# Performance work log

Hardware: AMD Instinct MI355X
Metric: run time of the kernel (lower is better)

## Reference

```python
import jax, jax.numpy as jnp
import numpy as np

B, S, E = 4, 2048, 1024
H = 16
HD = E // H  # head_dim = 64


def setup_inputs() -> dict:
    key = jax.random.key(0)
    ks = jax.random.split(key, 12)
    sc = 0.02
    return {
        "q_encodings": jax.random.normal(ks[0], (B, S, E), jnp.float32),
        "k_encodings": jax.random.normal(ks[1], (B, S, E), jnp.float32),
        "v_encodings": jax.random.normal(ks[2], (B, S, E), jnp.float32),
        # per-head q/k/v linear weights [H, HD, HD] and biases [H, HD]
        "Wq": jax.random.normal(ks[3], (H, HD, HD), jnp.float32) * sc,
        "bq": jax.random.normal(ks[4], (H, HD), jnp.float32) * sc,
        "Wk": jax.random.normal(ks[5], (H, HD, HD), jnp.float32) * sc,
        "bk": jax.random.normal(ks[6], (H, HD), jnp.float32) * sc,
        "Wv": jax.random.normal(ks[7], (H, HD, HD), jnp.float32) * sc,
        "bv": jax.random.normal(ks[8], (H, HD), jnp.float32) * sc,
        # output projection [E, E] + bias [E]
        "Wp": jax.random.normal(ks[9], (E, E), jnp.float32) * sc,
        "bp": jax.random.normal(ks[10], (E,), jnp.float32) * sc,
        "mask": 1,
    }


def reference(q_encodings, k_encodings, v_encodings, Wq, bq, Wk, bk, Wv, bv, Wp, bp, mask):
    b, s, e = q_encodings.shape
    h, hd, _ = Wq.shape
    split = lambda x: x.reshape(b, s, h, hd)  # per-head slices of n_embd
    # batched per-head linear projections (original loops over heads)
    Q = jnp.einsum('bshd,hde->bshe', split(q_encodings), Wq) + bq
    K = jnp.einsum('bshd,hde->bshe', split(k_encodings), Wk) + bk
    V = jnp.einsum('bshd,hde->bshe', split(v_encodings), Wv) + bv
    # scaled dot-product scores [B,H,S,S]; scale uses head_dim (Attention.n_embd)
    scores = jnp.einsum('bqhd,bkhd->bhqk', Q, K) / jnp.sqrt(jnp.float32(hd))
    if mask:  # static Python flag, matches torch `if mask:`
        causal = jnp.tril(jnp.ones((s, s), jnp.float32))
        scores = scores + jnp.where(causal == 0, jnp.float32(-jnp.inf), jnp.float32(0.0))
    attn = jax.nn.softmax(scores, axis=-1)
    ctx = jnp.einsum('bhqk,bkhd->bqhd', attn, V).reshape(b, s, e)
    return ctx @ Wp + bp
```

## Files before the change

### kernel.cpp

```cpp
#include <hip/hip_runtime.h>
#include <hip/hip_bf16.h>
#include <math.h>

typedef __bf16 bf16;
typedef __bf16 bf16x8 __attribute__((ext_vector_type(8)));
typedef float f32x4 __attribute__((ext_vector_type(4)));
typedef unsigned int u32x2 __attribute__((ext_vector_type(2)));

constexpr int B = 4, S = 2048, E = 1024, H = 16, HD = 64;

constexpr float QSCALE = 0.125f * 1.44269504088896340736f;
constexpr float DTHR = 11.5f;

static __device__ __forceinline__ float exp2_fast(float x) {
#if __has_builtin(__builtin_amdgcn_exp2f)
    return __builtin_amdgcn_exp2f(x);
#else
    float r; asm("v_exp_f32 %0, %1" : "=v"(r) : "v"(x)); return r;
#endif
}

static __device__ __forceinline__ unsigned pk_bf16(float a, float b) {
    union { bf16 h[2]; unsigned u; } r;
    r.h[0] = (bf16)a; r.h[1] = (bf16)b;
    return r.u;
}

static __device__ __forceinline__ float max3(float a, float b, float c) {
    return fmaxf(fmaxf(a, b), c);
}

static __device__ __forceinline__ void gl16(const void* g, void* l) {
    __builtin_amdgcn_global_load_lds(
        (__attribute__((address_space(1))) void*)g,
        (__attribute__((address_space(3))) void*)l,
        16, 0, 0);
}

__global__ __launch_bounds__(256) void prep_weights(
    const float* __restrict__ Wq, const float* __restrict__ Wk,
    const float* __restrict__ Wv, const float* __restrict__ Wp,
    bf16* __restrict__ Wt, bf16* __restrict__ Wpt)
{
    __shared__ float t[64][65];
    const int tid = threadIdx.x;
    const int x = blockIdx.x, y = blockIdx.y;
    if (y < 3) {
        const int h = x, p = y;
        const float* W = (p == 0) ? Wq : (p == 1) ? Wk : Wv;
        const float scale = (p == 0) ? QSCALE : 1.0f;
        #pragma unroll
        for (int i = 0; i < 16; ++i) {
            int idx = tid + i * 256;
            int d = idx >> 6, e = idx & 63;
            t[d][e] = W[(size_t)h * 4096 + d * 64 + e];
        }
        __syncthreads();
        bf16* dst = Wt + ((size_t)p * H + h) * 4096;
        #pragma unroll
        for (int i = 0; i < 16; ++i) {
            int idx = tid + i * 256;
            int e = idx >> 6, d = idx & 63;
            dst[e * 64 + d] = (bf16)(t[d][e] * scale);
        }
    } else {
        const int k0 = (y - 3) * 64, n0 = x * 64;
        #pragma unroll
        for (int i = 0; i < 16; ++i) {
            int idx = tid + i * 256;
            int r = idx >> 6, c = idx & 63;
            t[r][c] = Wp[(size_t)(k0 + r) * E + n0 + c];
        }
        __syncthreads();
        #pragma unroll
        for (int i = 0; i < 16; ++i) {
            int idx = tid + i * 256;
            int r = idx >> 6, c = idx & 63;
            Wpt[(size_t)(n0 + r) * E + k0 + c] = (bf16)t[c][r];
        }
    }
}

__global__ __launch_bounds__(256) void qkv_proj(
    const float* __restrict__ xq, const float* __restrict__ xk, const float* __restrict__ xv,
    const bf16* __restrict__ Wt,
    const float* __restrict__ bq, const float* __restrict__ bk, const float* __restrict__ bv,
    bf16* __restrict__ Qb, bf16* __restrict__ Kb, bf16* __restrict__ Vt)
{
    const int b = blockIdx.z, h = blockIdx.y, s0 = blockIdx.x * 128;
    const int tid = threadIdx.x;
    const int w = tid >> 6, l = tid & 63;
    const int l16 = l & 15, lg = l >> 4;
    const size_t bh = (size_t)b * H + h;

    __shared__ __align__(16) bf16 xs[128][64];
    __shared__ __align__(16) bf16 Wl[64][64];
    __shared__ __align__(16) bf16 ts[10240];

    const int r8 = l >> 3;
    const int wchunk = ((l & 7) ^ r8) * 8;

    for (int p = 0; p < 3; ++p) {
        const float* x    = (p == 0) ? xq : (p == 1) ? xk : xv;
        const float* bias = (p == 0) ? bq : (p == 1) ? bk : bv;
        const float  bsc  = (p == 0) ? QSCALE : 1.0f;

        __syncthreads();
        const bf16* wsrc = Wt + ((size_t)p * H + h) * 4096;
        #pragma unroll
        for (int i = 0; i < 2; ++i) {
            const int rb = 8 * (w + 4 * i);
            gl16(wsrc + (size_t)(rb + r8) * 64 + wchunk, &Wl[rb][0]);
        }
        #pragma unroll
        for (int i = 0; i < 4; ++i) {
            int idx = tid + i * 256;
            int r = idx >> 3, g = idx & 7;
            const float* src = &x[((size_t)b * S + s0 + r) * E + h * 64 + g * 8];
            float4 f0 = *(const float4*)src;
            float4 f1 = *(const float4*)(src + 4);
            union { bf16 h8[8]; uint4 u; } pk;
            pk.h8[0] = (bf16)f0.x; pk.h8[1] = (bf16)f0.y;
            pk.h8[2] = (bf16)f0.z; pk.h8[3] = (bf16)f0.w;
            pk.h8[4] = (bf16)f1.x; pk.h8[5] = (bf16)f1.y;
            pk.h8[6] = (bf16)f1.z; pk.h8[7] = (bf16)f1.w;
            *(uint4*)&xs[r][(g ^ (r & 7)) * 8] = pk.u;
        }
        __syncthreads();

        if (p < 2) {
            float bcol[4];
            #pragma unroll
            for (int ei = 0; ei < 4; ++ei)
                bcol[ei] = bias[h * 64 + ei * 16 + l16] * bsc;
            #pragma unroll
            for (int st = 0; st < 2; ++st) {
                const int srow = w * 32 + st * 16 + l16;
                bf16x8 a0 = *(const bf16x8*)&xs[srow][((lg    ) ^ (srow & 7)) * 8];
                bf16x8 a1 = *(const bf16x8*)&xs[srow][((4 + lg) ^ (srow & 7)) * 8];
                #pragma unroll
                for (int ei = 0; ei < 4; ++ei) {
                    const int erow = ei * 16 + l16;
                    bf16x8 b0 = *(const bf16x8*)&Wl[erow][((lg    ) ^ (erow & 7)) * 8];
                    bf16x8 b1 = *(const bf16x8*)&Wl[erow][((4 + lg) ^ (erow & 7)) * 8];
                    f32x4 acc = {0.f, 0.f, 0.f, 0.f};
                    acc = __builtin_amdgcn_mfma_f32_16x16x32_bf16(a0, b0, acc, 0, 0, 0);
                    acc = __builtin_amdgcn_mfma_f32_16x16x32_bf16(a1, b1, acc, 0, 0, 0);
                    #pragma unroll
                    for (int r = 0; r < 4; ++r)
                        ts[(w * 32 + st * 16 + 4 * lg + r) * 80 + ei * 16 + l16] =
                            (bf16)(acc[r] + bcol[ei]);
                }
            }
            __syncthreads();
            bf16* out = (p == 0) ? Qb : Kb;
            #pragma unroll
            for (int i = 0; i < 4; ++i) {
                int idx = tid + i * 256;
                int r = idx >> 3, g = idx & 7;
                uint4 v = *(const uint4*)&ts[r * 80 + g * 8];
                *(uint4*)(out + (bh * S + s0 + r) * 64 + g * 8) = v;
            }
        } else {
            float brow[4];
            #pragma unroll
            for (int r = 0; r < 4; ++r)
                brow[r] = bias[h * 64 + w * 16 + 4 * lg + r];
            const int erow = w * 16 + l16;
            bf16x8 a0 = *(const bf16x8*)&Wl[erow][((lg    ) ^ (erow & 7)) * 8];
            bf16x8 a1 = *(const bf16x8*)&Wl[erow][((4 + lg) ^ (erow & 7)) * 8];
            #pragma unroll
            for (int st = 0; st < 8; ++st) {
                const int srow = st * 16 + l16;
                bf16x8 b0 = *(const bf16x8*)&xs[srow][((lg    ) ^ (srow & 7)) * 8];
                bf16x8 b1 = *(const bf16x8*)&xs[srow][((4 + lg) ^ (srow & 7)) * 8];
                f32x4 acc = {0.f, 0.f, 0.f, 0.f};
                acc = __builtin_amdgcn_mfma_f32_16x16x32_bf16(a0, b0, acc, 0, 0, 0);
                acc = __builtin_amdgcn_mfma_f32_16x16x32_bf16(a1, b1, acc, 0, 0, 0);
                #pragma unroll
                for (int r = 0; r < 4; ++r)
                    ts[(w * 16 + 4 * lg + r) * 136 + st * 16 + l16] =
                        (bf16)(acc[r] + brow[r]);
            }
            __syncthreads();
            #pragma unroll
            for (int i = 0; i < 4; ++i) {
                int idx = tid + i * 256;
                int r = idx >> 4, g = idx & 15;
                uint4 v = *(const uint4*)&ts[r * 136 + g * 8];
                *(uint4*)(Vt + (bh * 64 + r) * S + s0 + g * 8) = v;
            }
        }
    }
}

__global__ __launch_bounds__(512) void attn(
    const bf16* __restrict__ Qb, const bf16* __restrict__ Kb,
    const bf16* __restrict__ Vt, bf16* __restrict__ ctx)
{
    const int lin = blockIdx.y * 8 + blockIdx.x;
    const int bh  = lin & 63;
    const int qt  = 15 - (lin >> 6);
    const int b = bh >> 4, h = bh & 15;
    const int tid = threadIdx.x;
    const int w = tid >> 6;
    const int l = tid & 63;
    const int l16 = l & 15, lg = l >> 4;

    __shared__ __align__(16) bf16 Kl[2][64][64];
    __shared__ __align__(16) bf16 Vl[2][64][64];
    __shared__ __align__(16) bf16 Pl[8][16][72];

    const bf16* Qp = Qb + (size_t)bh * S * 64;
    const bf16* Kp = Kb + (size_t)bh * S * 64;
    const bf16* Vp = Vt + (size_t)bh * 64 * S;

    const int str = tid >> 3;
    const int stc = tid & 7;
    const int sws = (stc ^ (str & 7)) * 8;

    int foff0[4], foff1[4];
    #pragma unroll
    for (int s = 0; s < 4; ++s) {
        foff0[s] = (16 * s + l16) * 64 + ((lg    ) ^ (l16 & 7)) * 8;
        foff1[s] = (16 * s + l16) * 64 + ((4 + lg) ^ (l16 & 7)) * 8;
    }
    bf16* Plw = &Pl[w][0][0];
    const int pwr = l16 * 72 + 4 * lg;
    const int prd = l16 * 72 + 8 * lg;

    const bf16 one_ = (bf16)1.0f;
    const bf16x8 ones = {one_, one_, one_, one_, one_, one_, one_, one_};

    const int qw0  = qt * 128 + w * 16;
    const int qabs = qw0 + l16;
    const int nt   = 2 * qt + 2;

    bf16x8 qf0 = *(const bf16x8*)(Qp + (size_t)qabs * 64 + lg * 8);
    bf16x8 qf1 = *(const bf16x8*)(Qp + (size_t)qabs * 64 + 32 + lg * 8);

    f32x4 o[4] = {};
    float m_run = -1e30f, l_run = 0.f;

    {
        uint4 kreg = *(const uint4*)(Kp + (size_t)str * 64 + stc * 8);
        uint4 vreg = *(const uint4*)(Vp + (size_t)str * S + stc * 8);
        *(uint4*)&Kl[0][str][sws] = kreg;
        *(uint4*)&Vl[0][str][sws] = vreg;
    }
    int cur = 0;
    for (int t = 0; t < nt; ++t) {
        __syncthreads();
        const bool pfv = (t + 1 < nt);
        uint4 kreg, vreg;
        if (pfv) {
            const int kv1 = (t + 1) * 64;
            kreg = *(const uint4*)(Kp + (size_t)(kv1 + str) * 64 + stc * 8);
            vreg = *(const uint4*)(Vp + (size_t)str * S + kv1 + stc * 8);
        }
        const int kv0 = t * 64;
        if (kv0 < qw0 + 16) {
            const bf16* Kbase = &Kl[cur][0][0];
            const bf16* Vbase = &Vl[cur][0][0];

            float p[16];
            __builtin_amdgcn_s_setprio(1);
            #pragma unroll
            for (int s = 0; s < 4; ++s) {
                f32x4 sc = {0.f, 0.f, 0.f, 0.f};
                bf16x8 ka = *(const bf16x8*)(Kbase + foff0[s]);
                bf16x8 kb = *(const bf16x8*)(Kbase + foff1[s]);
                sc = __builtin_amdgcn_mfma_f32_16x16x32_bf16(ka, qf0, sc, 0, 0, 0);
                sc = __builtin_amdgcn_mfma_f32_16x16x32_bf16(kb, qf1, sc, 0, 0, 0);
                p[4 * s + 0] = sc[0]; p[4 * s + 1] = sc[1];
                p[4 * s + 2] = sc[2]; p[4 * s + 3] = sc[3];
            }
            __builtin_amdgcn_s_setprio(0);

            if (kv0 + 63 > qw0) {
                #pragma unroll
                for (int i = 0; i < 16; ++i) {
                    const int kvloc = 16 * (i >> 2) + 4 * lg + (i & 3);
                    if (kv0 + kvloc > qabs) p[i] = -1e30f;
                }
            }

            const float a0 = max3(p[0],  p[1],  p[2]);
            const float a1 = max3(p[3],  p[4],  p[5]);
            const float a2 = max3(p[6],  p[7],  p[8]);
            const float a3 = max3(p[9],  p[10], p[11]);
            const float a4 = max3(p[12], p[13], p[14]);
            const float lmx = fmaxf(max3(a0, a1, a2), max3(a3, a4, p[15]));
            if (!__all(lmx <= m_run + DTHR)) {
                float mx = fmaxf(lmx, __shfl_xor(lmx, 16));
                mx = fmaxf(mx, __shfl_xor(mx, 32));
                const float m_new = fmaxf(m_run, mx);
                const float corr = exp2_fast(m_run - m_new);
                l_run *= corr;
                #pragma unroll
                for (int ds = 0; ds < 4; ++ds) {
                    o[ds][0] *= corr; o[ds][1] *= corr;
                    o[ds][2] *= corr; o[ds][3] *= corr;
                }
                m_run = m_new;
            }
            #pragma unroll
            for (int i = 0; i < 16; ++i) p[i] = exp2_fast(p[i] - m_run);

            #pragma unroll
            for (int s = 0; s < 4; ++s) {
                u32x2 pw;
                pw[0] = pk_bf16(p[4 * s + 0], p[4 * s + 1]);
                pw[1] = pk_bf16(p[4 * s + 2], p[4 * s + 3]);
                *(u32x2*)(Plw + pwr + 16 * s) = pw;
            }
            asm volatile("s_waitcnt lgkmcnt(0)" ::: "memory");
            bf16x8 pf0 = *(const bf16x8*)(Plw + prd);
            bf16x8 pf1 = *(const bf16x8*)(Plw + prd + 32);

            __builtin_amdgcn_s_setprio(1);
            f32x4 o5 = {0.f, 0.f, 0.f, 0.f};
            o5 = __builtin_amdgcn_mfma_f32_16x16x32_bf16(ones, pf0, o5, 0, 0, 0);
            o5 = __builtin_amdgcn_mfma_f32_16x16x32_bf16(ones, pf1, o5, 0, 0, 0);
            #pragma unroll
            for (int ds = 0; ds < 4; ++ds) {
                bf16x8 v0 = *(const bf16x8*)(Vbase + foff0[ds]);
                bf16x8 v1 = *(const bf16x8*)(Vbase + foff1[ds]);
                o[ds] = __builtin_amdgcn_mfma_f32_16x16x32_bf16(v0, pf0, o[ds], 0, 0, 0);
                o[ds] = __builtin_amdgcn_mfma_f32_16x16x32_bf16(v1, pf1, o[ds], 0, 0, 0);
            }
            __builtin_amdgcn_s_setprio(0);
            l_run += o5[0];
        }
        if (pfv) {
            *(uint4*)&Kl[cur ^ 1][str][sws] = kreg;
            *(uint4*)&Vl[cur ^ 1][str][sws] = vreg;
        }
        cur ^= 1;
    }

    const float il = 1.0f / l_run;
    bf16* crow = ctx + ((size_t)b * S + qabs) * E + h * 64;
    #pragma unroll
    for (int ds = 0; ds < 4; ++ds) {
        u32x2 pw;
        pw[0] = pk_bf16(o[ds][0] * il, o[ds][1] * il);
        pw[1] = pk_bf16(o[ds][2] * il, o[ds][3] * il);
        *(u32x2*)(crow + 16 * ds + 4 * lg) = pw;
    }
}

__global__ __launch_bounds__(256) void out_gemm(
    const bf16* __restrict__ A, const bf16* __restrict__ Bt,
    const float* __restrict__ bp, float* __restrict__ C)
{
    const int lin = blockIdx.y * 8 + blockIdx.x;
    const int c   = lin & 7;
    const int k   = lin >> 3;
    const int n0  = (k & 7) * 128;
    const int m0  = (((k >> 3) << 3) | c) * 128;
    const int tid = threadIdx.x;
    const int w = tid >> 6, l = tid & 63;
    const int l16 = l & 15, lg = l >> 4;
    const int wm = w >> 1, wn = w & 1;

    __shared__ __align__(16) bf16 Al[2][128][64];
    __shared__ __align__(16) bf16 Bl[2][128][64];

    f32x4 acc[4][4] = {};

    const int r8 = l >> 3;
    const int chunk = ((l & 7) ^ r8) * 8;

    #pragma unroll
    for (int i = 0; i < 4; ++i) {
        const int rb = 8 * w + 32 * i;
        gl16(A  + (size_t)(m0 + rb + r8) * E + chunk, &Al[0][rb][0]);
        gl16(Bt + (size_t)(n0 + rb + r8) * E + chunk, &Bl[0][rb][0]);
    }

    int cur = 0;
    for (int k0 = 0; k0 < E; k0 += 64) {
        __syncthreads();
        if (k0 + 64 < E) {
            #pragma unroll
            for (int i = 0; i < 4; ++i) {
                const int rb = 8 * w + 32 * i;
                gl16(A  + (size_t)(m0 + rb + r8) * E + k0 + 64 + chunk,
                     &Al[cur ^ 1][rb][0]);
                gl16(Bt + (size_t)(n0 + rb + r8) * E + k0 + 64 + chunk,
                     &Bl[cur ^ 1][rb][0]);
            }
        }
        #pragma unroll
        for (int ks = 0; ks < 2; ++ks) {
            bf16x8 af[4], bfr[4];
            #pragma unroll
            for (int mi = 0; mi < 4; ++mi) {
                int r = wm * 64 + mi * 16 + l16;
                af[mi] = *(const bf16x8*)&Al[cur][r][((ks * 4 + lg) ^ (r & 7)) * 8];
            }
            #pragma unroll
            for (int ni = 0; ni < 4; ++ni) {
                int r = wn * 64 + ni * 16 + l16;
                bfr[ni] = *(const bf16x8*)&Bl[cur][r][((ks * 4 + lg) ^ (r & 7)) * 8];
            }
            #pragma unroll
            for (int mi = 0; mi < 4; ++mi)
                #pragma unroll
                for (int ni = 0; ni < 4; ++ni)
                    acc[mi][ni] = __builtin_amdgcn_mfma_f32_16x16x32_bf16(
                        af[mi], bfr[ni], acc[mi][ni], 0, 0, 0);
        }
        cur ^= 1;
    }

    #pragma unroll
    for (int ni = 0; ni < 4; ++ni) {
        const int col = n0 + wn * 64 + ni * 16 + l16;
        const float bias = bp[col];
        #pragma unroll
        for (int mi = 0; mi < 4; ++mi) {
            #pragma unroll
            for (int e = 0; e < 4; ++e) {
                int row = m0 + wm * 64 + mi * 16 + 4 * lg + e;
                C[(size_t)row * E + col] = acc[mi][ni][e] + bias;
            }
        }
    }
}

extern "C" void kernel_launch(void* const* d_in, const int* in_sizes, int n_in,
                              void* d_out, int out_size, void* d_ws, size_t ws_size,
                              hipStream_t stream)
{
    const float* xq = (const float*)d_in[0];
    const float* xk = (const float*)d_in[1];
    const float* xv = (const float*)d_in[2];
    const float* Wq = (const float*)d_in[3];
    const float* bq = (const float*)d_in[4];
    const float* Wk = (const float*)d_in[5];
    const float* bk = (const float*)d_in[6];
    const float* Wv = (const float*)d_in[7];
    const float* bv = (const float*)d_in[8];
    const float* Wp = (const float*)d_in[9];
    const float* bp = (const float*)d_in[10];
    float* out = (float*)d_out;

    char* ws = (char*)d_ws;
    const size_t sz_bhse = (size_t)B * H * S * HD;
    bf16* Qb  = (bf16*)ws;  ws += sz_bhse * 2;
    bf16* Kb  = (bf16*)ws;  ws += sz_bhse * 2;
    bf16* Vtw = (bf16*)ws;  ws += sz_bhse * 2;
    bf16* ctx = (bf16*)ws;  ws += (size_t)B * S * E * 2;
    bf16* Wpt = (bf16*)ws;  ws += (size_t)E * E * 2;
    bf16* Wt3 = (bf16*)ws;  ws += (size_t)3 * H * HD * HD * 2;

    prep_weights<<<dim3(16, 19), 256, 0, stream>>>(Wq, Wk, Wv, Wp, Wt3, Wpt);
    qkv_proj<<<dim3(S / 128, H, B), 256, 0, stream>>>(xq, xk, xv, Wt3,
                                                      bq, bk, bv, Qb, Kb, Vtw);
    attn<<<dim3(8, 128), 512, 0, stream>>>(Qb, Kb, Vtw, ctx);
    out_gemm<<<dim3(E / 128, (B * S) / 128), 256, 0, stream>>>(ctx, Wpt, bp, out);
}
```

Before: 108.9 us.

## Software-pipeline attention loop so QK of next tile overlaps softmax/PV of previous

Restructures the flash-attention inner loop into a two-stage software pipeline, unrolled by two. The QK^T MFMAs for tile t+1 are issued before the softmax and PV of tile t, and K and V are staged into separate LDS slots at different phases. The goal is to hide the softmax/exp latency and the LDS round trip behind matrix-core work. In exchange it adds register pressure from two live score arrays and a more intricate buffer-slot and sync schedule, with a final epilogue SM_PV for the last tile.

```diff
diff --git a/kernel.cpp b/kernel.cpp
--- a/kernel.cpp
+++ b/kernel.cpp
@@ -241,6 +241,7 @@
 
     f32x4 o[4] = {};
     float m_run = -1e30f, l_run = 0.f;
+    float pA[16], pB[16];
 
     {
         uint4 kreg = *(const uint4*)(Kp + (size_t)str * 64 + stc * 8);
@@ -248,96 +249,100 @@
         *(uint4*)&Kl[0][str][sws] = kreg;
         *(uint4*)&Vl[0][str][sws] = vreg;
     }
-    int cur = 0;
-    for (int t = 0; t < nt; ++t) {
-        __syncthreads();
-        const bool pfv = (t + 1 < nt);
-        uint4 kreg, vreg;
-        if (pfv) {
+
+#define QK_MASK(tt, kslot, P) do {                                           \
+    const bf16* Kbase_ = &Kl[kslot][0][0];                                   \
+    __builtin_amdgcn_s_setprio(1);                                           \
+    _Pragma("unroll") for (int s_ = 0; s_ < 4; ++s_) {                       \
+        f32x4 sc_ = {0.f, 0.f, 0.f, 0.f};                                    \
+        bf16x8 ka_ = *(const bf16x8*)(Kbase_ + foff0[s_]);                   \
+        bf16x8 kb_ = *(const bf16x8*)(Kbase_ + foff1[s_]);                   \
+        sc_ = __builtin_amdgcn_mfma_f32_16x16x32_bf16(ka_, qf0, sc_, 0,0,0); \
+        sc_ = __builtin_amdgcn_mfma_f32_16x16x32_bf16(kb_, qf1, sc_, 0,0,0); \
+        P[4*s_+0]=sc_[0]; P[4*s_+1]=sc_[1]; P[4*s_+2]=sc_[2]; P[4*s_+3]=sc_[3]; } \
+    __builtin_amdgcn_s_setprio(0);                                           \
+    const int kv0_ = (tt) * 64;                                              \
+    if (kv0_ + 63 > qw0) {                                                   \
+        _Pragma("unroll") for (int i_ = 0; i_ < 16; ++i_) {                  \
+            const int kvloc_ = 16 * (i_ >> 2) + 4 * lg + (i_ & 3);           \
+            if (kv0_ + kvloc_ > qabs) P[i_] = -1e30f; } }                    \
+} while (0)
+
+#define SM_PV(vslot, P) do {                                                 \
+    const bf16* Vbase_ = &Vl[vslot][0][0];                                   \
+    const float a0_ = max3(P[0],  P[1],  P[2]);                              \
+    const float a1_ = max3(P[3],  P[4],  P[5]);                              \
+    const float a2_ = max3(P[6],  P[7],  P[8]);                              \
+    const float a3_ = max3(P[9],  P[10], P[11]);                             \
+    const float a4_ = max3(P[12], P[13], P[14]);                             \
+    const float lmx_ = fmaxf(max3(a0_, a1_, a2_), max3(a3_, a4_, P[15]));    \
+    if (!__all(lmx_ <= m_run + DTHR)) {                                      \
+        float mx_ = fmaxf(lmx_, __shfl_xor(lmx_, 16));                       \
+        mx_ = fmaxf(mx_, __shfl_xor(mx_, 32));                               \
+        const float m_new_ = fmaxf(m_run, mx_);                              \
+        const float corr_ = exp2_fast(m_run - m_new_);                       \
+        l_run *= corr_;                                                      \
+        _Pragma("unroll") for (int d_ = 0; d_ < 4; ++d_) {                   \
+            o[d_][0] *= corr_; o[d_][1] *= corr_;                            \
+            o[d_][2] *= corr_; o[d_][3] *= corr_; }                          \
+        m_run = m_new_; }                                                    \
+    _Pragma("unroll") for (int i_ = 0; i_ < 16; ++i_)                        \
+        P[i_] = exp2_fast(P[i_] - m_run);                                    \
+    _Pragma("unroll") for (int s_ = 0; s_ < 4; ++s_) {                       \
+        u32x2 pw_;                                                           \
+        pw_[0] = pk_bf16(P[4*s_+0], P[4*s_+1]);                              \
+        pw_[1] = pk_bf16(P[4*s_+2], P[4*s_+3]);                              \
+        *(u32x2*)(Plw + pwr + 16 * s_) = pw_; }                              \
+    asm volatile("s_waitcnt lgkmcnt(0)" ::: "memory");                       \
+    bf16x8 pf0_ = *(const bf16x8*)(Plw + prd);                               \
+    bf16x8 pf1_ = *(const bf16x8*)(Plw + prd + 32);                          \
+    __builtin_amdgcn_s_setprio(1);                                           \
+    f32x4 o5_ = {0.f, 0.f, 0.f, 0.f};                                        \
+    o5_ = __builtin_amdgcn_mfma_f32_16x16x32_bf16(ones, pf0_, o5_, 0,0,0);   \
+    o5_ = __builtin_amdgcn_mfma_f32_16x16x32_bf16(ones, pf1_, o5_, 0,0,0);   \
+    _Pragma("unroll") for (int d_ = 0; d_ < 4; ++d_) {                       \
+        bf16x8 v0_ = *(const bf16x8*)(Vbase_ + foff0[d_]);                   \
+        bf16x8 v1_ = *(const bf16x8*)(Vbase_ + foff1[d_]);                   \
+        o[d_] = __builtin_amdgcn_mfma_f32_16x16x32_bf16(v0_, pf0_, o[d_], 0,0,0); \
+        o[d_] = __builtin_amdgcn_mfma_f32_16x16x32_bf16(v1_, pf1_, o[d_], 0,0,0); } \
+    __builtin_amdgcn_s_setprio(0);                                           \
+    l_run += o5_[0];                                                         \
+} while (0)
+
+    uint4 vhA, vhB;
+    #pragma unroll 1
+    for (int t = 0; t < nt; t += 2) {
+        __syncthreads();
+        uint4 kregA;
+        {
             const int kv1 = (t + 1) * 64;
-            kreg = *(const uint4*)(Kp + (size_t)(kv1 + str) * 64 + stc * 8);
-            vreg = *(const uint4*)(Vp + (size_t)str * S + kv1 + stc * 8);
-        }
-        const int kv0 = t * 64;
-        if (kv0 < qw0 + 16) {
-            const bf16* Kbase = &Kl[cur][0][0];
-            const bf16* Vbase = &Vl[cur][0][0];
-
-            float p[16];
-            __builtin_amdgcn_s_setprio(1);
-            #pragma unroll
-            for (int s = 0; s < 4; ++s) {
-                f32x4 sc = {0.f, 0.f, 0.f, 0.f};
-                bf16x8 ka = *(const bf16x8*)(Kbase + foff0[s]);
-                bf16x8 kb = *(const bf16x8*)(Kbase + foff1[s]);
-                sc = __builtin_amdgcn_mfma_f32_16x16x32_bf16(ka, qf0, sc, 0, 0, 0);
-                sc = __builtin_amdgcn_mfma_f32_16x16x32_bf16(kb, qf1, sc, 0, 0, 0);
-                p[4 * s + 0] = sc[0]; p[4 * s + 1] = sc[1];
-                p[4 * s + 2] = sc[2]; p[4 * s + 3] = sc[3];
-            }
-            __builtin_amdgcn_s_setprio(0);
-
-            if (kv0 + 63 > qw0) {
-                #pragma unroll
-                for (int i = 0; i < 16; ++i) {
-                    const int kvloc = 16 * (i >> 2) + 4 * lg + (i & 3);
-                    if (kv0 + kvloc > qabs) p[i] = -1e30f;
-                }
-            }
-
-            const float a0 = max3(p[0],  p[1],  p[2]);
-            const float a1 = max3(p[3],  p[4],  p[5]);
-            const float a2 = max3(p[6],  p[7],  p[8]);
-            const float a3 = max3(p[9],  p[10], p[11]);
-            const float a4 = max3(p[12], p[13], p[14]);
-            const float lmx = fmaxf(max3(a0, a1, a2), max3(a3, a4, p[15]));
-            if (!__all(lmx <= m_run + DTHR)) {
-                float mx = fmaxf(lmx, __shfl_xor(lmx, 16));
-                mx = fmaxf(mx, __shfl_xor(mx, 32));
-                const float m_new = fmaxf(m_run, mx);
-                const float corr = exp2_fast(m_run - m_new);
-                l_run *= corr;
-                #pragma unroll
-                for (int ds = 0; ds < 4; ++ds) {
-                    o[ds][0] *= corr; o[ds][1] *= corr;
-                    o[ds][2] *= corr; o[ds][3] *= corr;
-                }
-                m_run = m_new;
-            }
-            #pragma unroll
-            for (int i = 0; i < 16; ++i) p[i] = exp2_fast(p[i] - m_run);
-
-            #pragma unroll
-            for (int s = 0; s < 4; ++s) {
-                u32x2 pw;
-                pw[0] = pk_bf16(p[4 * s + 0], p[4 * s + 1]);
-                pw[1] = pk_bf16(p[4 * s + 2], p[4 * s + 3]);
-                *(u32x2*)(Plw + pwr + 16 * s) = pw;
-            }
-            asm volatile("s_waitcnt lgkmcnt(0)" ::: "memory");
-            bf16x8 pf0 = *(const bf16x8*)(Plw + prd);
-            bf16x8 pf1 = *(const bf16x8*)(Plw + prd + 32);
-
-            __builtin_amdgcn_s_setprio(1);
-            f32x4 o5 = {0.f, 0.f, 0.f, 0.f};
-            o5 = __builtin_amdgcn_mfma_f32_16x16x32_bf16(ones, pf0, o5, 0, 0, 0);
-            o5 = __builtin_amdgcn_mfma_f32_16x16x32_bf16(ones, pf1, o5, 0, 0, 0);
-            #pragma unroll
-            for (int ds = 0; ds < 4; ++ds) {
-                bf16x8 v0 = *(const bf16x8*)(Vbase + foff0[ds]);
-                bf16x8 v1 = *(const bf16x8*)(Vbase + foff1[ds]);
-                o[ds] = __builtin_amdgcn_mfma_f32_16x16x32_bf16(v0, pf0, o[ds], 0, 0, 0);
-                o[ds] = __builtin_amdgcn_mfma_f32_16x16x32_bf16(v1, pf1, o[ds], 0, 0, 0);
-            }
-            __builtin_amdgcn_s_setprio(0);
-            l_run += o5[0];
-        }
-        if (pfv) {
-            *(uint4*)&Kl[cur ^ 1][str][sws] = kreg;
-            *(uint4*)&Vl[cur ^ 1][str][sws] = vreg;
-        }
-        cur ^= 1;
-    }
+            kregA = *(const uint4*)(Kp + (size_t)(kv1 + str) * 64 + stc * 8);
+            vhA   = *(const uint4*)(Vp + (size_t)str * S + kv1 + stc * 8);
+        }
+        const bool doT = (t * 64 < qw0 + 16);
+        if (doT) QK_MASK(t, 0, pA);
+        if (t > 0 && (t - 1) * 64 < qw0 + 16) SM_PV(1, pB);
+        *(uint4*)&Kl[1][str][sws] = kregA;
+        if (t > 0) *(uint4*)&Vl[0][str][sws] = vhB;
+
+        __syncthreads();
+        const bool more = (t + 2 < nt);
+        uint4 kregB;
+        if (more) {
+            const int kv2 = (t + 2) * 64;
+            kregB = *(const uint4*)(Kp + (size_t)(kv2 + str) * 64 + stc * 8);
+            vhB   = *(const uint4*)(Vp + (size_t)str * S + kv2 + stc * 8);
+        }
+        if ((t + 1) * 64 < qw0 + 16) QK_MASK(t + 1, 1, pB);
+        if (doT) SM_PV(0, pA);
+        if (more) *(uint4*)&Kl[0][str][sws] = kregB;
+        *(uint4*)&Vl[1][str][sws] = vhA;
+    }
+    __syncthreads();
+    if ((nt - 1) * 64 < qw0 + 16) SM_PV(1, pB);
+
+#undef QK_MASK
+#undef SM_PV
 
     const float il = 1.0f / l_run;
     bf16* crow = ctx + ((size_t)b * S + qabs) * E + h * 64;
```

After: 126.0 us (median of 2 runs). 15.7% more time.
